# Kernel tuning notes

Hardware: AMD Instinct MI355X
Metric: run time of the kernel (lower is better)

Reference implementation:

```python
import jax, jax.numpy as jnp
import numpy as np

N = 100000      # nodes
E = 1600000     # edges (avg degree 16)
IN, H, H4, OUT = 2, 128, 32, 64
B = 1000        # batch_size for final view


def setup_inputs() -> dict:
    key = jax.random.key(0)
    ks = jax.random.split(key, 16)
    w = lambda k, s: (jax.random.normal(k, s, jnp.float32) * (1.0 / np.sqrt(s[0])))
    return {
        "x": jax.random.normal(ks[0], (N, IN), jnp.float32),
        "edge_index": jax.random.randint(ks[1], (2, E), 0, N, dtype=jnp.int32),
        "batch_size": B,
        "W1": w(ks[2], (IN, H)),  "b1": jnp.zeros((H,), jnp.float32),
        "W2": w(ks[3], (H, H)),   "b2": jnp.zeros((H,), jnp.float32),
        "W3": w(ks[4], (H, H4)),  "b3": jnp.zeros((H4,), jnp.float32),
        "W4": w(ks[5], (H4, H4)), "b4": jnp.zeros((H4,), jnp.float32),
        "W5": w(ks[6], (H4, OUT)),"b5": jnp.zeros((OUT,), jnp.float32),
        "Wl": w(ks[7], (OUT, 1)), "bl": jnp.zeros((1,), jnp.float32),
    }


def gcn_conv(x, src, dst, W, b, n):
    # PyG GCNConv: add self-loops, symmetric degree normalization, scatter-add.
    h = x @ W  # [N, F]
    deg = jax.ops.segment_sum(jnp.ones(src.shape[0], h.dtype), dst,
                              num_segments=n) + 1.0  # +1 for self-loop
    dinv = jax.lax.rsqrt(deg)  # deg >= 1, no inf
    norm = dinv[src] * dinv[dst]  # [E]
    agg = jax.ops.segment_sum(h[src] * norm[:, None], dst, num_segments=n)
    agg = agg + h * (dinv * dinv)[:, None]  # self-loop contribution
    return agg + b


def reference(x, edge_index, batch_size, W1, b1, W2, b2, W3, b3, W4, b4, W5, b5, Wl, bl):
    x = x.reshape(-1, 2)
    n = x.shape[0]
    src, dst = edge_index[0], edge_index[1]
    for W, b in ((W1, b1), (W2, b2), (W3, b3), (W4, b4), (W5, b5)):
        x = jax.nn.relu(gcn_conv(x, src, dst, W, b, n))
    x = x @ Wl + bl  # [N, 1]
    return x.reshape(batch_size, -1)
```

## Files before the change

### kernel.cpp

```cpp
#include <hip/hip_runtime.h>
#include <math.h>


static inline int cdiv(int a, int b) { return (a + b - 1) / b; }

__global__ void zero_i32(int* __restrict__ p, int n) {
    int i = blockIdx.x * 256 + threadIdx.x;
    if (i < n) p[i] = 0;
}

__global__ void count_kernel(const int* __restrict__ dst, int* __restrict__ cnt, int E) {
    int e = blockIdx.x * 256 + threadIdx.x;
    if (e < E) atomicAdd(&cnt[dst[e]], 1);
}

__global__ void scan1(const int* __restrict__ cnt, int* __restrict__ off,
                      int* __restrict__ bsum, int n) {
    __shared__ int sm[256];
    int i = blockIdx.x * 256 + threadIdx.x;
    int v = (i < n) ? cnt[i] : 0;
    sm[threadIdx.x] = v;
    __syncthreads();
    for (int ofs = 1; ofs < 256; ofs <<= 1) {
        int t = (threadIdx.x >= (unsigned)ofs) ? sm[threadIdx.x - ofs] : 0;
        __syncthreads();
        sm[threadIdx.x] += t;
        __syncthreads();
    }
    if (i < n) off[i] = sm[threadIdx.x];
    if (threadIdx.x == 255) bsum[blockIdx.x] = sm[255];
}

__global__ void scan2(const int* __restrict__ bsum, int* __restrict__ bpre,
                      int nb, int* __restrict__ off, int N, int E) {
    __shared__ int sm[512];
    int t = threadIdx.x;
    sm[t] = (t < nb) ? bsum[t] : 0;
    __syncthreads();
    for (int ofs = 1; ofs < 512; ofs <<= 1) {
        int v = (t >= ofs) ? sm[t - ofs] : 0;
        __syncthreads();
        sm[t] += v;
        __syncthreads();
    }
    if (t < nb) bpre[t] = sm[t] - bsum[t];
    if (t == 0) off[N] = E;
}

__global__ void scan3_fused(const int* __restrict__ cnt, const int* __restrict__ bpre,
                            int* __restrict__ off, int* __restrict__ cursor,
                            const float* __restrict__ x, float* __restrict__ dinv,
                            float* __restrict__ xs, int n) {
    int i = blockIdx.x * 256 + threadIdx.x;
    if (i < n) {
        int c = cnt[i];
        int o = off[i] - c + bpre[blockIdx.x];
        off[i] = o;
        cursor[i] = o;
        float dv = 1.0f / sqrtf((float)c + 1.0f);
        dinv[i] = dv;
        float2 xv = *reinterpret_cast<const float2*>(x + 2 * (size_t)i);
        *reinterpret_cast<float2*>(xs + 2 * (size_t)i) = float2{dv * xv.x, dv * xv.y};
    }
}

__global__ __launch_bounds__(256) void fill_ranged(const int* __restrict__ src,
                                                   const int* __restrict__ dst,
                                                   int* __restrict__ cursor,
                                                   int* __restrict__ csr,
                                                   int E, int N, int echunk) {
    int cls = blockIdx.x & 7;
    int chunk = blockIdx.x >> 3;
    int per = (N + 7) >> 3;
    int lo = cls * per;
    int hi = lo + per; if (hi > N) hi = N;
    int e0 = chunk * echunk;
    int e1 = e0 + echunk; if (e1 > E) e1 = E;
    for (int e = e0 + (int)threadIdx.x; e < e1; e += 256) {
        int d = dst[e];
        if (d >= lo && d < hi) {
            int p = atomicAdd(&cursor[d], 1);
            csr[p] = src[e];
        }
    }
}

__global__ __launch_bounds__(256) void agg2_kernel(const float* __restrict__ xs,
                                                   const int* __restrict__ off,
                                                   const int* __restrict__ csr,
                                                   const float* __restrict__ dinv,
                                                   float* __restrict__ out, int n) {
    int v = blockIdx.x * 256 + threadIdx.x;
    if (v >= n) return;
    float a0 = 0.f, a1 = 0.f;
    int e0 = off[v], e1 = off[v + 1];
    for (int e = e0; e < e1; e++) {
        int s = csr[e];
        float2 q = *reinterpret_cast<const float2*>(xs + 2 * (size_t)s);
        a0 += q.x;
        a1 += q.y;
    }
    float dv = dinv[v];
    float2 xv = *reinterpret_cast<const float2*>(xs + 2 * (size_t)v);
    *reinterpret_cast<float2*>(out + 2 * (size_t)v) =
        float2{dv * (a0 + xv.x), dv * (a1 + xv.y)};
}

template <bool BR, bool PS>
__global__ __launch_bounds__(256) void agg128x_kernel(const float* __restrict__ hc,
                                                      const int* __restrict__ off,
                                                      const int* __restrict__ csr,
                                                      const float* __restrict__ dinv,
                                                      const float* __restrict__ bias,
                                                      float* __restrict__ outc, int n) {
    int cls = blockIdx.x & 7;
    int chunk = cls >> 1;
    int half = cls & 1;
    int n2 = (n + 1) >> 1;
    int lo = half * n2;
    int hi = lo + n2; if (hi > n) hi = n;

    const float* __restrict__ h = hc + (size_t)chunk * n * 32;
    float* __restrict__ out = outc + (size_t)chunk * n * 32;

    int tid = threadIdx.x;
    int lane = tid & 63;
    int sl = lane & 7;
    int subbase = lane & ~7;
    int wave = tid >> 6;
    int v = lo + (blockIdx.x >> 3) * 32 + wave * 8 + (lane >> 3);
    if (v >= hi) return;

    int start = off[v];
    int end = off[v + 1];

    float4 acc = {0.f, 0.f, 0.f, 0.f};

    for (int base = start; base < end; base += 16) {
        int m = end - base;
        if (m > 16) m = 16;
        int idxA = (sl < m) ? csr[base + sl] : 0;
        int idxB = (8 + sl < m) ? csr[base + 8 + sl] : 0;
        if (m == 16) {
            float4 hb[16];
#pragma unroll
            for (int u = 0; u < 16; u++) {
                int s = __shfl((u < 8) ? idxA : idxB, subbase + (u & 7));
                hb[u] = *reinterpret_cast<const float4*>(h + (size_t)s * 32 + sl * 4);
            }
#pragma unroll
            for (int u = 0; u < 16; u++) {
                acc.x += hb[u].x; acc.y += hb[u].y; acc.z += hb[u].z; acc.w += hb[u].w;
            }
        } else {
            int ma = (m < 8) ? m : 8;
            int i = 0;
            for (; i + 4 <= ma; i += 4) {
                float4 hb[4];
#pragma unroll
                for (int u = 0; u < 4; u++) {
                    int s = __shfl(idxA, subbase + i + u);
                    hb[u] = *reinterpret_cast<const float4*>(h + (size_t)s * 32 + sl * 4);
                }
#pragma unroll
                for (int u = 0; u < 4; u++) {
                    acc.x += hb[u].x; acc.y += hb[u].y; acc.z += hb[u].z; acc.w += hb[u].w;
                }
            }
            if (i + 2 <= ma) {
                int s0 = __shfl(idxA, subbase + i);
                int s1 = __shfl(idxA, subbase + i + 1);
                float4 h0 = *reinterpret_cast<const float4*>(h + (size_t)s0 * 32 + sl * 4);
                float4 h1 = *reinterpret_cast<const float4*>(h + (size_t)s1 * 32 + sl * 4);
                acc.x += h0.x + h1.x; acc.y += h0.y + h1.y;
                acc.z += h0.z + h1.z; acc.w += h0.w + h1.w;
                i += 2;
            }
            if (i < ma) {
                int s0 = __shfl(idxA, subbase + i);
                float4 h0 = *reinterpret_cast<const float4*>(h + (size_t)s0 * 32 + sl * 4);
                acc.x += h0.x; acc.y += h0.y; acc.z += h0.z; acc.w += h0.w;
            }
            if (m > 8) {
                int mb = m - 8;
                int j = 0;
                for (; j + 4 <= mb; j += 4) {
                    float4 hb[4];
#pragma unroll
                    for (int u = 0; u < 4; u++) {
                        int s = __shfl(idxB, subbase + j + u);
                        hb[u] = *reinterpret_cast<const float4*>(h + (size_t)s * 32 + sl * 4);
                    }
#pragma unroll
                    for (int u = 0; u < 4; u++) {
                        acc.x += hb[u].x; acc.y += hb[u].y; acc.z += hb[u].z; acc.w += hb[u].w;
                    }
                }
                if (j + 2 <= mb) {
                    int s0 = __shfl(idxB, subbase + j);
                    int s1 = __shfl(idxB, subbase + j + 1);
                    float4 h0 = *reinterpret_cast<const float4*>(h + (size_t)s0 * 32 + sl * 4);
                    float4 h1 = *reinterpret_cast<const float4*>(h + (size_t)s1 * 32 + sl * 4);
                    acc.x += h0.x + h1.x; acc.y += h0.y + h1.y;
                    acc.z += h0.z + h1.z; acc.w += h0.w + h1.w;
                    j += 2;
                }
                if (j < mb) {
                    int s0 = __shfl(idxB, subbase + j);
                    float4 h0 = *reinterpret_cast<const float4*>(h + (size_t)s0 * 32 + sl * 4);
                    acc.x += h0.x; acc.y += h0.y; acc.z += h0.z; acc.w += h0.w;
                }
            }
        }
    }

    float dv = dinv[v];
    float4 hv = *reinterpret_cast<const float4*>(h + (size_t)v * 32 + sl * 4);
    float o0 = dv * (acc.x + hv.x);
    float o1 = dv * (acc.y + hv.y);
    float o2 = dv * (acc.z + hv.z);
    float o3 = dv * (acc.w + hv.w);
    if constexpr (BR) {
        float4 b = *reinterpret_cast<const float4*>(bias + chunk * 32 + sl * 4);
        o0 = fmaxf(o0 + b.x, 0.f);
        o1 = fmaxf(o1 + b.y, 0.f);
        o2 = fmaxf(o2 + b.z, 0.f);
        o3 = fmaxf(o3 + b.w, 0.f);
    }
    if constexpr (PS) {
        o0 *= dv; o1 *= dv; o2 *= dv; o3 *= dv;
    }
    *reinterpret_cast<float4*>(out + (size_t)v * 32 + sl * 4) = float4{o0, o1, o2, o3};
}

template <bool BR, bool PS>
__global__ __launch_bounds__(256) void agg32_kernel(const float* __restrict__ h,
                                                    const int* __restrict__ off,
                                                    const int* __restrict__ csr,
                                                    const float* __restrict__ dinv,
                                                    const float* __restrict__ bias,
                                                    float* __restrict__ out, int n) {
    int tid = threadIdx.x;
    int lane = tid & 63;
    int sl = lane & 7;
    int subbase = lane & ~7;
    int wave = tid >> 6;
    int v = blockIdx.x * 32 + wave * 8 + (lane >> 3);
    if (v >= n) return;

    int start = off[v];
    int end = off[v + 1];

    float4 acc = {0.f, 0.f, 0.f, 0.f};

    for (int base = start; base < end; base += 16) {
        int m = end - base;
        if (m > 16) m = 16;
        int idxA = (sl < m) ? csr[base + sl] : 0;
        int idxB = (8 + sl < m) ? csr[base + 8 + sl] : 0;
        if (m == 16) {
            float4 hb[16];
#pragma unroll
            for (int u = 0; u < 16; u++) {
                int s = __shfl((u < 8) ? idxA : idxB, subbase + (u & 7));
                hb[u] = *reinterpret_cast<const float4*>(h + (size_t)s * 32 + sl * 4);
            }
#pragma unroll
            for (int u = 0; u < 16; u++) {
                acc.x += hb[u].x; acc.y += hb[u].y; acc.z += hb[u].z; acc.w += hb[u].w;
            }
        } else {
            int ma = (m < 8) ? m : 8;
            int i = 0;
            for (; i + 4 <= ma; i += 4) {
                float4 hb[4];
#pragma unroll
                for (int u = 0; u < 4; u++) {
                    int s = __shfl(idxA, subbase + i + u);
                    hb[u] = *reinterpret_cast<const float4*>(h + (size_t)s * 32 + sl * 4);
                }
#pragma unroll
                for (int u = 0; u < 4; u++) {
                    acc.x += hb[u].x; acc.y += hb[u].y; acc.z += hb[u].z; acc.w += hb[u].w;
                }
            }
            if (i + 2 <= ma) {
                int s0 = __shfl(idxA, subbase + i);
                int s1 = __shfl(idxA, subbase + i + 1);
                float4 h0 = *reinterpret_cast<const float4*>(h + (size_t)s0 * 32 + sl * 4);
                float4 h1 = *reinterpret_cast<const float4*>(h + (size_t)s1 * 32 + sl * 4);
                acc.x += h0.x + h1.x; acc.y += h0.y + h1.y;
                acc.z += h0.z + h1.z; acc.w += h0.w + h1.w;
                i += 2;
            }
            if (i < ma) {
                int s0 = __shfl(idxA, subbase + i);
                float4 h0 = *reinterpret_cast<const float4*>(h + (size_t)s0 * 32 + sl * 4);
                acc.x += h0.x; acc.y += h0.y; acc.z += h0.z; acc.w += h0.w;
            }
            if (m > 8) {
                int mb = m - 8;
                int j = 0;
                for (; j + 4 <= mb; j += 4) {
                    float4 hb[4];
#pragma unroll
                    for (int u = 0; u < 4; u++) {
                        int s = __shfl(idxB, subbase + j + u);
                        hb[u] = *reinterpret_cast<const float4*>(h + (size_t)s * 32 + sl * 4);
                    }
#pragma unroll
                    for (int u = 0; u < 4; u++) {
                        acc.x += hb[u].x; acc.y += hb[u].y; acc.z += hb[u].z; acc.w += hb[u].w;
                    }
                }
                if (j + 2 <= mb) {
                    int s0 = __shfl(idxB, subbase + j);
                    int s1 = __shfl(idxB, subbase + j + 1);
                    float4 h0 = *reinterpret_cast<const float4*>(h + (size_t)s0 * 32 + sl * 4);
                    float4 h1 = *reinterpret_cast<const float4*>(h + (size_t)s1 * 32 + sl * 4);
                    acc.x += h0.x + h1.x; acc.y += h0.y + h1.y;
                    acc.z += h0.z + h1.z; acc.w += h0.w + h1.w;
                    j += 2;
                }
                if (j < mb) {
                    int s0 = __shfl(idxB, subbase + j);
                    float4 h0 = *reinterpret_cast<const float4*>(h + (size_t)s0 * 32 + sl * 4);
                    acc.x += h0.x; acc.y += h0.y; acc.z += h0.z; acc.w += h0.w;
                }
            }
        }
    }

    float dv = dinv[v];
    float4 hv = *reinterpret_cast<const float4*>(h + (size_t)v * 32 + sl * 4);
    float o0 = dv * (acc.x + hv.x);
    float o1 = dv * (acc.y + hv.y);
    float o2 = dv * (acc.z + hv.z);
    float o3 = dv * (acc.w + hv.w);
    if constexpr (BR) {
        float4 b = *reinterpret_cast<const float4*>(bias + sl * 4);
        o0 = fmaxf(o0 + b.x, 0.f);
        o1 = fmaxf(o1 + b.y, 0.f);
        o2 = fmaxf(o2 + b.z, 0.f);
        o3 = fmaxf(o3 + b.w, 0.f);
    }
    if constexpr (PS) {
        o0 *= dv; o1 *= dv; o2 *= dv; o3 *= dv;
    }
    *reinterpret_cast<float4*>(out + (size_t)v * 32 + sl * 4) = float4{o0, o1, o2, o3};
}

template <int K, int F, bool BR, bool PS, int CIN = 0, int COUT = 0>
__global__ __launch_bounds__(256, 4) void gemm_tiled(const float* __restrict__ x,
                                                     const float* __restrict__ W,
                                                     const float* __restrict__ bias,
                                                     const float* __restrict__ dinv,
                                                     float* __restrict__ h, int n) {
    constexpr int KC = 32;
    constexpr int KCP = 36;
    constexpr int ROWS = 64;
    constexpr int TPC = F / 4;
    constexpr int RT = 256 / TPC;
    constexpr int RPT = ROWS / RT;
    static_assert(K % KC == 0, "K must be a multiple of 32");

    __shared__ float Ws[KC * F];
    __shared__ float Xs[ROWS * KCP];

    const int tid = threadIdx.x;
    const int cb = (tid % TPC) * 4;
    const int tr = tid / TPC;
    const int row0 = blockIdx.x * ROWS;

    float acc[RPT][4];
#pragma unroll
    for (int r = 0; r < RPT; r++)
#pragma unroll
        for (int j = 0; j < 4; j++) acc[r][j] = 0.f;

#pragma unroll 1
    for (int k0 = 0; k0 < K; k0 += KC) {
        __syncthreads();
        {
            int r = tid >> 2;
            int kk = (tid & 3) * 8;
            int gr = row0 + r;
            float4 v0 = {0.f, 0.f, 0.f, 0.f}, v1 = {0.f, 0.f, 0.f, 0.f};
            if (gr < n) {
                if constexpr (CIN == 32) {
                    const float* xb = x + (size_t)(k0 >> 5) * n * 32 + (size_t)gr * 32 + kk;
                    v0 = *reinterpret_cast<const float4*>(xb);
                    v1 = *reinterpret_cast<const float4*>(xb + 4);
                } else {
                    v0 = *reinterpret_cast<const float4*>(x + (size_t)gr * K + k0 + kk);
                    v1 = *reinterpret_cast<const float4*>(x + (size_t)gr * K + k0 + kk + 4);
                }
            }
            *reinterpret_cast<float4*>(&Xs[r * KCP + kk]) = v0;
            *reinterpret_cast<float4*>(&Xs[r * KCP + kk + 4]) = v1;
        }
        for (int i = tid; i < KC * F / 4; i += 256) {
            *reinterpret_cast<float4*>(&Ws[i * 4]) =
                *reinterpret_cast<const float4*>(W + (size_t)k0 * F + i * 4);
        }
        __syncthreads();

#pragma unroll 4
        for (int kk4 = 0; kk4 < KC; kk4 += 4) {
            float4 xr[RPT];
#pragma unroll
            for (int r = 0; r < RPT; r++)
                xr[r] = *reinterpret_cast<const float4*>(&Xs[(tr * RPT + r) * KCP + kk4]);
#pragma unroll
            for (int j = 0; j < 4; j++) {
                float4 w = *reinterpret_cast<const float4*>(&Ws[(kk4 + j) * F + cb]);
#pragma unroll
                for (int r = 0; r < RPT; r++) {
                    float xv = (j == 0) ? xr[r].x : (j == 1) ? xr[r].y
                             : (j == 2) ? xr[r].z : xr[r].w;
                    acc[r][0] += xv * w.x;
                    acc[r][1] += xv * w.y;
                    acc[r][2] += xv * w.z;
                    acc[r][3] += xv * w.w;
                }
            }
        }
    }

    float4 b = float4{0.f, 0.f, 0.f, 0.f};
    if constexpr (BR) b = *reinterpret_cast<const float4*>(bias + cb);
#pragma unroll
    for (int r = 0; r < RPT; r++) {
        int row = row0 + tr * RPT + r;
        if (row < n) {
            float o0 = acc[r][0], o1 = acc[r][1], o2 = acc[r][2], o3 = acc[r][3];
            if constexpr (BR) {
                o0 = fmaxf(o0 + b.x, 0.f);
                o1 = fmaxf(o1 + b.y, 0.f);
                o2 = fmaxf(o2 + b.z, 0.f);
                o3 = fmaxf(o3 + b.w, 0.f);
            }
            if constexpr (PS) {
                float dv = dinv[row];
                o0 *= dv; o1 *= dv; o2 *= dv; o3 *= dv;
            }
            if constexpr (COUT == 32) {
                float* hb = h + (size_t)(cb >> 5) * n * 32 + (size_t)row * 32 + (cb & 31);
                *reinterpret_cast<float4*>(hb) = float4{o0, o1, o2, o3};
            } else {
                *reinterpret_cast<float4*>(&h[(size_t)row * F + cb]) = float4{o0, o1, o2, o3};
            }
        }
    }
}

__global__ __launch_bounds__(256, 4) void gemm_final(const float* __restrict__ x,
                                                     const float* __restrict__ W,
                                                     const float* __restrict__ bias,
                                                     const float* __restrict__ Wl,
                                                     const float* __restrict__ bl,
                                                     float* __restrict__ out, int n) {
    constexpr int K = 32, F = 64;
    constexpr int KC = 32;
    constexpr int KCP = 36;
    constexpr int ROWS = 64;
    constexpr int TPC = F / 4;
    constexpr int RT = 256 / TPC;
    constexpr int RPT = ROWS / RT;

    __shared__ float Ws[KC * F];
    __shared__ float Xs[ROWS * KCP];
    __shared__ float wl[F];

    const int tid = threadIdx.x;
    if (tid < F) wl[tid] = Wl[tid];
    const int cb = (tid % TPC) * 4;
    const int tr = tid / TPC;
    const int row0 = blockIdx.x * ROWS;

    float acc[RPT][4];
#pragma unroll
    for (int r = 0; r < RPT; r++)
#pragma unroll
        for (int j = 0; j < 4; j++) acc[r][j] = 0.f;

    {
        {
            int r = tid >> 2;
            int kk = (tid & 3) * 8;
            int gr = row0 + r;
            float4 v0 = {0.f, 0.f, 0.f, 0.f}, v1 = {0.f, 0.f, 0.f, 0.f};
            if (gr < n) {
                v0 = *reinterpret_cast<const float4*>(x + (size_t)gr * K + kk);
                v1 = *reinterpret_cast<const float4*>(x + (size_t)gr * K + kk + 4);
            }
            *reinterpret_cast<float4*>(&Xs[r * KCP + kk]) = v0;
            *reinterpret_cast<float4*>(&Xs[r * KCP + kk + 4]) = v1;
        }
        for (int i = tid; i < KC * F / 4; i += 256) {
            *reinterpret_cast<float4*>(&Ws[i * 4]) =
                *reinterpret_cast<const float4*>(W + i * 4);
        }
        __syncthreads();

#pragma unroll 4
        for (int kk4 = 0; kk4 < KC; kk4 += 4) {
            float4 xr[RPT];
#pragma unroll
            for (int r = 0; r < RPT; r++)
                xr[r] = *reinterpret_cast<const float4*>(&Xs[(tr * RPT + r) * KCP + kk4]);
#pragma unroll
            for (int j = 0; j < 4; j++) {
                float4 w = *reinterpret_cast<const float4*>(&Ws[(kk4 + j) * F + cb]);
#pragma unroll
                for (int r = 0; r < RPT; r++) {
                    float xv = (j == 0) ? xr[r].x : (j == 1) ? xr[r].y
                             : (j == 2) ? xr[r].z : xr[r].w;
                    acc[r][0] += xv * w.x;
                    acc[r][1] += xv * w.y;
                    acc[r][2] += xv * w.z;
                    acc[r][3] += xv * w.w;
                }
            }
        }
    }

    float4 b = *reinterpret_cast<const float4*>(bias + cb);
    float4 w = *reinterpret_cast<const float4*>(&wl[cb]);
    float blv = bl[0];
#pragma unroll
    for (int r = 0; r < RPT; r++) {
        int row = row0 + tr * RPT + r;
        float o0 = fmaxf(acc[r][0] + b.x, 0.f);
        float o1 = fmaxf(acc[r][1] + b.y, 0.f);
        float o2 = fmaxf(acc[r][2] + b.z, 0.f);
        float o3 = fmaxf(acc[r][3] + b.w, 0.f);
        float partial = o0 * w.x + o1 * w.y + o2 * w.z + o3 * w.w;
        partial += __shfl_xor(partial, 8, 16);
        partial += __shfl_xor(partial, 4, 16);
        partial += __shfl_xor(partial, 2, 16);
        partial += __shfl_xor(partial, 1, 16);
        if ((tid & 15) == 0 && row < n) out[row] = partial + blv;
    }
}

template <int K, int F, bool BR, bool PS>
__global__ __launch_bounds__(256, 4) void gemm_small(const float* __restrict__ x,
                                                     const float* __restrict__ W,
                                                     const float* __restrict__ bias,
                                                     const float* __restrict__ dinv,
                                                     float* __restrict__ h, int n) {
    constexpr int TPR = F / 4;
    constexpr int ROWS = 256 / TPR;
    __shared__ float Ws[K * F];
    for (int i = threadIdx.x; i < K * F; i += 256) Ws[i] = W[i];
    __syncthreads();

    int tid = threadIdx.x;
    int cb = (tid % TPR) * 4;
    int r = blockIdx.x * ROWS + tid / TPR;
    if (r >= n) return;

    const float* xr = x + (size_t)r * K;
    float a0 = 0.f, a1 = 0.f, a2 = 0.f, a3 = 0.f;
#pragma unroll
    for (int k = 0; k < K; k++) {
        float xv = xr[k];
        float4 w = *reinterpret_cast<const float4*>(&Ws[k * F + cb]);
        a0 += xv * w.x; a1 += xv * w.y; a2 += xv * w.z; a3 += xv * w.w;
    }
    if constexpr (BR) {
        float4 b = *reinterpret_cast<const float4*>(bias + cb);
        a0 = fmaxf(a0 + b.x, 0.f);
        a1 = fmaxf(a1 + b.y, 0.f);
        a2 = fmaxf(a2 + b.z, 0.f);
        a3 = fmaxf(a3 + b.w, 0.f);
    }
    if constexpr (PS) {
        float dv = dinv[r];
        a0 *= dv; a1 *= dv; a2 *= dv; a3 *= dv;
    }
    *reinterpret_cast<float4*>(&h[(size_t)r * F + cb]) = float4{a0, a1, a2, a3};
}

extern "C" void kernel_launch(void* const* d_in, const int* in_sizes, int n_in,
                              void* d_out, int out_size, void* d_ws, size_t ws_size,
                              hipStream_t stream) {
    const float* x = (const float*)d_in[0];
    const int* ei = (const int*)d_in[1];
    const float* W1 = (const float*)d_in[3];
    const float* b1 = (const float*)d_in[4];
    const float* W2 = (const float*)d_in[5];
    const float* b2 = (const float*)d_in[6];
    const float* W3 = (const float*)d_in[7];
    const float* b3 = (const float*)d_in[8];
    const float* W4 = (const float*)d_in[9];
    const float* b4 = (const float*)d_in[10];
    const float* W5 = (const float*)d_in[11];
    const float* b5 = (const float*)d_in[12];
    const float* Wl = (const float*)d_in[13];
    const float* bl = (const float*)d_in[14];

    const int N = in_sizes[0] / 2;
    const int E = in_sizes[1] / 2;
    const int* src = ei;
    const int* dst = ei + E;

    char* wp = (char*)d_ws;
    auto alloc = [&](size_t bytes) -> void* {
        void* p = wp;
        wp += ((bytes + 255) / 256) * 256;
        return p;
    };
    int* cnt = (int*)alloc((size_t)N * 4);
    int* off = (int*)alloc((size_t)(N + 1) * 4);
    int* cursor = (int*)alloc((size_t)N * 4);
    int* bsum = (int*)alloc(512 * 4);
    int* bpre = (int*)alloc(512 * 4);
    int* csr = (int*)alloc((size_t)E * 4);
    float* dinv = (float*)alloc((size_t)N * 4);
    float* xs2 = (float*)alloc((size_t)N * 2 * 4);
    float* t2 = (float*)alloc((size_t)N * 2 * 4);
    float* bufA = (float*)alloc((size_t)N * 128 * 4);
    float* bufB = (float*)alloc((size_t)N * 128 * 4);

    const int gN = cdiv(N, 256);
    const int gE = cdiv(E, 256);
    const int nb = gN;
    const int gT = cdiv(N, 64);

    const int NCHUNK = 128;
    const int echunk = cdiv(E, NCHUNK);
    const int gR = 8 * NCHUNK;

    const int gX = 8 * cdiv((N + 1) / 2, 32);

    zero_i32<<<gN, 256, 0, stream>>>(cnt, N);
    count_kernel<<<gE, 256, 0, stream>>>(dst, cnt, E);
    scan1<<<nb, 256, 0, stream>>>(cnt, off, bsum, N);
    scan2<<<1, 512, 0, stream>>>(bsum, bpre, nb, off, N, E);
    scan3_fused<<<nb, 256, 0, stream>>>(cnt, bpre, off, cursor, x, dinv, xs2, N);
    fill_ranged<<<gR, 256, 0, stream>>>(src, dst, cursor, csr, E, N, echunk);

    agg2_kernel<<<gN, 256, 0, stream>>>(xs2, off, csr, dinv, t2, N);
    gemm_small<2, 128, true, true><<<cdiv(N, 8), 256, 0, stream>>>(t2, W1, b1, dinv, bufA, N);
    gemm_tiled<128, 128, false, false, 0, 32><<<gT, 256, 0, stream>>>(bufA, W2, nullptr, nullptr, bufB, N);
    agg128x_kernel<true, true><<<gX, 256, 0, stream>>>(bufB, off, csr, dinv, b2, bufA, N);
    gemm_tiled<128, 32, false, false, 32, 0><<<gT, 256, 0, stream>>>(bufA, W3, nullptr, nullptr, bufB, N);
    agg32_kernel<true, true><<<cdiv(N, 32), 256, 0, stream>>>(bufB, off, csr, dinv, b3, bufA, N);
    gemm_tiled<32, 32, false, false, 0, 0><<<gT, 256, 0, stream>>>(bufA, W4, nullptr, nullptr, bufB, N);
    agg32_kernel<true, true><<<cdiv(N, 32), 256, 0, stream>>>(bufB, off, csr, dinv, b4, bufA, N);
    agg32_kernel<false, false><<<cdiv(N, 32), 256, 0, stream>>>(bufA, off, csr, dinv, nullptr, bufB, N);
    gemm_final<<<gT, 256, 0, stream>>>(bufB, W5, b5, Wl, bl, (float*)d_out, N);
}
```

Measured before the change: 530.5 us.

## Split 32-wide feature layers into 8-column chunks for cache-friendly aggregation

Stores the 32-feature hidden activations as four column chunks of 8 floats each (chunk-major), and rewrites the 32-wide aggregation to process one chunk per block class, also splitting nodes into halves. Each gather then touches a 32-byte row inside a 3.2 MB chunk array instead of a 12.8 MB array, aiming to keep the gathered working set in cache. This mirrors the earlier 128-wide chunked kernel. The GEMMs gain matching chunked input and output addressing. The cost is four times as many narrower scalar gathers per edge, and the CSR indices are re-read once per chunk.

Measured after the change: 572.3 us. 1.08x slower.

```diff
diff --git a/kernel.cpp b/kernel.cpp
--- a/kernel.cpp
+++ b/kernel.cpp
@@ -234,24 +234,34 @@
 }
 
 template <bool BR, bool PS>
-__global__ __launch_bounds__(256) void agg32_kernel(const float* __restrict__ h,
-                                                    const int* __restrict__ off,
-                                                    const int* __restrict__ csr,
-                                                    const float* __restrict__ dinv,
-                                                    const float* __restrict__ bias,
-                                                    float* __restrict__ out, int n) {
+__global__ __launch_bounds__(256) void agg32x_kernel(const float* __restrict__ hc,
+                                                     const int* __restrict__ off,
+                                                     const int* __restrict__ csr,
+                                                     const float* __restrict__ dinv,
+                                                     const float* __restrict__ bias,
+                                                     float* __restrict__ outc, int n) {
+    int cls = blockIdx.x & 7;
+    int chunk = cls >> 1;
+    int half = cls & 1;
+    int n2 = (n + 1) >> 1;
+    int lo = half * n2;
+    int hi = lo + n2; if (hi > n) hi = n;
+
+    const float* __restrict__ h = hc + (size_t)chunk * n * 8;
+    float* __restrict__ out = outc + (size_t)chunk * n * 8;
+
     int tid = threadIdx.x;
     int lane = tid & 63;
     int sl = lane & 7;
     int subbase = lane & ~7;
     int wave = tid >> 6;
-    int v = blockIdx.x * 32 + wave * 8 + (lane >> 3);
-    if (v >= n) return;
+    int v = lo + (blockIdx.x >> 3) * 32 + wave * 8 + (lane >> 3);
+    if (v >= hi) return;
 
     int start = off[v];
     int end = off[v + 1];
 
-    float4 acc = {0.f, 0.f, 0.f, 0.f};
+    float acc = 0.f;
 
     for (int base = start; base < end; base += 16) {
         int m = end - base;
@@ -259,95 +269,74 @@
         int idxA = (sl < m) ? csr[base + sl] : 0;
         int idxB = (8 + sl < m) ? csr[base + 8 + sl] : 0;
         if (m == 16) {
-            float4 hb[16];
+            float hb[16];
 #pragma unroll
             for (int u = 0; u < 16; u++) {
                 int s = __shfl((u < 8) ? idxA : idxB, subbase + (u & 7));
-                hb[u] = *reinterpret_cast<const float4*>(h + (size_t)s * 32 + sl * 4);
-            }
-#pragma unroll
-            for (int u = 0; u < 16; u++) {
-                acc.x += hb[u].x; acc.y += hb[u].y; acc.z += hb[u].z; acc.w += hb[u].w;
-            }
+                hb[u] = h[(size_t)s * 8 + sl];
+            }
+#pragma unroll
+            for (int u = 0; u < 16; u++) acc += hb[u];
         } else {
             int ma = (m < 8) ? m : 8;
             int i = 0;
             for (; i + 4 <= ma; i += 4) {
-                float4 hb[4];
+                float hb[4];
 #pragma unroll
                 for (int u = 0; u < 4; u++) {
                     int s = __shfl(idxA, subbase + i + u);
-                    hb[u] = *reinterpret_cast<const float4*>(h + (size_t)s * 32 + sl * 4);
-                }
-#pragma unroll
-                for (int u = 0; u < 4; u++) {
-                    acc.x += hb[u].x; acc.y += hb[u].y; acc.z += hb[u].z; acc.w += hb[u].w;
-                }
+                    hb[u] = h[(size_t)s * 8 + sl];
+                }
+#pragma unroll
+                for (int u = 0; u < 4; u++) acc += hb[u];
             }
             if (i + 2 <= ma) {
                 int s0 = __shfl(idxA, subbase + i);
                 int s1 = __shfl(idxA, subbase + i + 1);
-                float4 h0 = *reinterpret_cast<const float4*>(h + (size_t)s0 * 32 + sl * 4);
-                float4 h1 = *reinterpret_cast<const float4*>(h + (size_t)s1 * 32 + sl * 4);
-                acc.x += h0.x + h1.x; acc.y += h0.y + h1.y;
-                acc.z += h0.z + h1.z; acc.w += h0.w + h1.w;
+                acc += h[(size_t)s0 * 8 + sl] + h[(size_t)s1 * 8 + sl];
                 i += 2;
             }
             if (i < ma) {
                 int s0 = __shfl(idxA, subbase + i);
-                float4 h0 = *reinterpret_cast<const float4*>(h + (size_t)s0 * 32 + sl * 4);
-                acc.x += h0.x; acc.y += h0.y; acc.z += h0.z; acc.w += h0.w;
+                acc += h[(size_t)s0 * 8 + sl];
             }
             if (m > 8) {
                 int mb = m - 8;
                 int j = 0;
                 for (; j + 4 <= mb; j += 4) {
-                    float4 hb[4];
+                    float hb[4];
 #pragma unroll
                     for (int u = 0; u < 4; u++) {
                         int s = __shfl(idxB, subbase + j + u);
-                        hb[u] = *reinterpret_cast<const float4*>(h + (size_t)s * 32 + sl * 4);
+                        hb[u] = h[(size_t)s * 8 + sl];
                     }
 #pragma unroll
-                    for (int u = 0; u < 4; u++) {
-                        acc.x += hb[u].x; acc.y += hb[u].y; acc.z += hb[u].z; acc.w += hb[u].w;
-                    }
+                    for (int u = 0; u < 4; u++) acc += hb[u];
                 }
                 if (j + 2 <= mb) {
                     int s0 = __shfl(idxB, subbase + j);
                     int s1 = __shfl(idxB, subbase + j + 1);
-                    float4 h0 = *reinterpret_cast<const float4*>(h + (size_t)s0 * 32 + sl * 4);
-                    float4 h1 = *reinterpret_cast<const float4*>(h + (size_t)s1 * 32 + sl * 4);
-                    acc.x += h0.x + h1.x; acc.y += h0.y + h1.y;
-                    acc.z += h0.z + h1.z; acc.w += h0.w + h1.w;
+                    acc += h[(size_t)s0 * 8 + sl] + h[(size_t)s1 * 8 + sl];
                     j += 2;
                 }
                 if (j < mb) {
                     int s0 = __shfl(idxB, subbase + j);
-                    float4 h0 = *reinterpret_cast<const float4*>(h + (size_t)s0 * 32 + sl * 4);
-                    acc.x += h0.x; acc.y += h0.y; acc.z += h0.z; acc.w += h0.w;
+                    acc += h[(size_t)s0 * 8 + sl];
                 }
             }
         }
     }
 
     float dv = dinv[v];
-    float4 hv = *reinterpret_cast<const float4*>(h + (size_t)v * 32 + sl * 4);
-    float o0 = dv * (acc.x + hv.x);
-    float o1 = dv * (acc.y + hv.y);
-    float o2 = dv * (acc.z + hv.z);
-    float o3 = dv * (acc.w + hv.w);
+    float hv = h[(size_t)v * 8 + sl];
+    float o = dv * (acc + hv);
     if constexpr (BR) {
-        float4 b = *reinterpret_cast<const float4*>(bias + sl * 4);
-        o0 = fmaxf(o0 + b.x, 0.f);
-        o1 = fmaxf(o1 + b.y, 0.f);
-        o2 = fmaxf(o2 + b.z, 0.f);
-        o3 = fmaxf(o3 + b.w, 0.f);
+        o = fmaxf(o + bias[chunk * 8 + sl], 0.f);
     }
     if constexpr (PS) {
-        o0 *= dv; o1 *= dv; o2 *= dv; o3 *= dv;
-    }
-    *reinterpret_cast<float4*>(out + (size_t)v * 32 + sl * 4) = float4{o0, o1, o2, o3};
+        o *= dv;
+    }
+    out[(size_t)v * 8 + sl] = o;
 }
 
 template <int K, int F, bool BR, bool PS, int CIN = 0, int COUT = 0>
@@ -391,6 +380,10 @@
                     const float* xb = x + (size_t)(k0 >> 5) * n * 32 + (size_t)gr * 32 + kk;
                     v0 = *reinterpret_cast<const float4*>(xb);
                     v1 = *reinterpret_cast<const float4*>(xb + 4);
+                } else if constexpr (CIN == 8) {
+                    const float* xb = x + (size_t)((k0 + kk) >> 3) * n * 8 + (size_t)gr * 8;
+                    v0 = *reinterpret_cast<const float4*>(xb);
+                    v1 = *reinterpret_cast<const float4*>(xb + 4);
                 } else {
                     v0 = *reinterpret_cast<const float4*>(x + (size_t)gr * K + k0 + kk);
                     v1 = *reinterpret_cast<const float4*>(x + (size_t)gr * K + k0 + kk + 4);
@@ -446,6 +439,9 @@
             }
             if constexpr (COUT == 32) {
                 float* hb = h + (size_t)(cb >> 5) * n * 32 + (size_t)row * 32 + (cb & 31);
+                *reinterpret_cast<float4*>(hb) = float4{o0, o1, o2, o3};
+            } else if constexpr (COUT == 8) {
+                float* hb = h + (size_t)(cb >> 3) * n * 8 + (size_t)row * 8 + (cb & 7);
                 *reinterpret_cast<float4*>(hb) = float4{o0, o1, o2, o3};
             } else {
                 *reinterpret_cast<float4*>(&h[(size_t)row * F + cb]) = float4{o0, o1, o2, o3};
@@ -491,8 +487,9 @@
             int gr = row0 + r;
             float4 v0 = {0.f, 0.f, 0.f, 0.f}, v1 = {0.f, 0.f, 0.f, 0.f};
             if (gr < n) {
-                v0 = *reinterpret_cast<const float4*>(x + (size_t)gr * K + kk);
-                v1 = *reinterpret_cast<const float4*>(x + (size_t)gr * K + kk + 4);
+                const float* xb = x + (size_t)(kk >> 3) * n * 8 + (size_t)gr * 8;
+                v0 = *reinterpret_cast<const float4*>(xb);
+                v1 = *reinterpret_cast<const float4*>(xb + 4);
             }
             *reinterpret_cast<float4*>(&Xs[r * KCP + kk]) = v0;
             *reinterpret_cast<float4*>(&Xs[r * KCP + kk + 4]) = v1;
@@ -646,10 +643,10 @@
     gemm_small<2, 128, true, true><<<cdiv(N, 8), 256, 0, stream>>>(t2, W1, b1, dinv, bufA, N);
     gemm_tiled<128, 128, false, false, 0, 32><<<gT, 256, 0, stream>>>(bufA, W2, nullptr, nullptr, bufB, N);
     agg128x_kernel<true, true><<<gX, 256, 0, stream>>>(bufB, off, csr, dinv, b2, bufA, N);
-    gemm_tiled<128, 32, false, false, 32, 0><<<gT, 256, 0, stream>>>(bufA, W3, nullptr, nullptr, bufB, N);
-    agg32_kernel<true, true><<<cdiv(N, 32), 256, 0, stream>>>(bufB, off, csr, dinv, b3, bufA, N);
-    gemm_tiled<32, 32, false, false, 0, 0><<<gT, 256, 0, stream>>>(bufA, W4, nullptr, nullptr, bufB, N);
-    agg32_kernel<true, true><<<cdiv(N, 32), 256, 0, stream>>>(bufB, off, csr, dinv, b4, bufA, N);
-    agg32_kernel<false, false><<<cdiv(N, 32), 256, 0, stream>>>(bufA, off, csr, dinv, nullptr, bufB, N);
+    gemm_tiled<128, 32, false, false, 32, 8><<<gT, 256, 0, stream>>>(bufA, W3, nullptr, nullptr, bufB, N);
+    agg32x_kernel<true, true><<<gX, 256, 0, stream>>>(bufB, off, csr, dinv, b3, bufA, N);
+    gemm_tiled<32, 32, false, false, 8, 8><<<gT, 256, 0, stream>>>(bufA, W4, nullptr, nullptr, bufB, N);
+    agg32x_kernel<true, true><<<gX, 256, 0, stream>>>(bufB, off, csr, dinv, b4, bufA, N);
+    agg32x_kernel<false, false><<<gX, 256, 0, stream>>>(bufA, off, csr, dinv, nullptr, bufB, N);
     gemm_final<<<gT, 256, 0, stream>>>(bufB, W5, b5, Wl, bl, (float*)d_out, N);
 }
```

## Partition CSR neighbors into source octants for phased L2-local gathers in agg128

Applied to the files above, without the earlier changes.

The CSR build now buckets each destination's neighbors by which eighth of the node range their source falls in, using per-node 8-way counters and cursors. The 128-wide aggregation kernel uses these buckets to sweep the octants in order, with each 8-lane group handling 9 nodes at once. The goal is to keep the gathered source rows for the current phase inside a smaller working set that fits in cache. The cost is 8x larger count and cursor arrays, more atomics and scan work, shorter 4-wide inner batches with less memory-level parallelism per node, and higher register pressure.

Result: slower. 630.4 us (+18.8%).

```diff
diff --git a/kernel.cpp b/kernel.cpp
--- a/kernel.cpp
+++ b/kernel.cpp
@@ -9,16 +9,27 @@
     if (i < n) p[i] = 0;
 }
 
-__global__ void count_kernel(const int* __restrict__ dst, int* __restrict__ cnt, int E) {
+__global__ void count_q8(const int* __restrict__ src, const int* __restrict__ dst,
+                         int* __restrict__ cnt8, int E, int q1) {
     int e = blockIdx.x * 256 + threadIdx.x;
-    if (e < E) atomicAdd(&cnt[dst[e]], 1);
-}
-
-__global__ void scan1(const int* __restrict__ cnt, int* __restrict__ off,
-                      int* __restrict__ bsum, int n) {
+    if (e < E) {
+        int s = src[e];
+        int q = (s >= q1) + (s >= 2 * q1) + (s >= 3 * q1) + (s >= 4 * q1) +
+                (s >= 5 * q1) + (s >= 6 * q1) + (s >= 7 * q1);
+        atomicAdd(&cnt8[dst[e] * 8 + q], 1);
+    }
+}
+
+__global__ void scan1q8(const int* __restrict__ cnt8, int* __restrict__ off,
+                        int* __restrict__ bsum, int n) {
     __shared__ int sm[256];
     int i = blockIdx.x * 256 + threadIdx.x;
-    int v = (i < n) ? cnt[i] : 0;
+    int v = 0;
+    if (i < n) {
+        int4 a = *reinterpret_cast<const int4*>(cnt8 + 8 * (size_t)i);
+        int4 b = *reinterpret_cast<const int4*>(cnt8 + 8 * (size_t)i + 4);
+        v = a.x + a.y + a.z + a.w + b.x + b.y + b.z + b.w;
+    }
     sm[threadIdx.x] = v;
     __syncthreads();
     for (int ofs = 1; ofs < 256; ofs <<= 1) {
@@ -47,16 +58,28 @@
     if (t == 0) off[N] = E;
 }
 
-__global__ void scan3_fused(const int* __restrict__ cnt, const int* __restrict__ bpre,
-                            int* __restrict__ off, int* __restrict__ cursor,
-                            const float* __restrict__ x, float* __restrict__ dinv,
-                            float* __restrict__ xs, int n) {
+__global__ void scan3_fused8(const int* __restrict__ cnt8, const int* __restrict__ bpre,
+                             int* __restrict__ off, int* __restrict__ cur8,
+                             const float* __restrict__ x, float* __restrict__ dinv,
+                             float* __restrict__ xs, int n) {
     int i = blockIdx.x * 256 + threadIdx.x;
     if (i < n) {
-        int c = cnt[i];
+        int4 a = *reinterpret_cast<const int4*>(cnt8 + 8 * (size_t)i);
+        int4 b = *reinterpret_cast<const int4*>(cnt8 + 8 * (size_t)i + 4);
+        int c = a.x + a.y + a.z + a.w + b.x + b.y + b.z + b.w;
         int o = off[i] - c + bpre[blockIdx.x];
         off[i] = o;
-        cursor[i] = o;
+        int4 ca, cb;
+        ca.x = o;
+        ca.y = ca.x + a.x;
+        ca.z = ca.y + a.y;
+        ca.w = ca.z + a.z;
+        cb.x = ca.w + a.w;
+        cb.y = cb.x + b.x;
+        cb.z = cb.y + b.y;
+        cb.w = cb.z + b.z;
+        *reinterpret_cast<int4*>(cur8 + 8 * (size_t)i) = ca;
+        *reinterpret_cast<int4*>(cur8 + 8 * (size_t)i + 4) = cb;
         float dv = 1.0f / sqrtf((float)c + 1.0f);
         dinv[i] = dv;
         float2 xv = *reinterpret_cast<const float2*>(x + 2 * (size_t)i);
@@ -64,11 +87,11 @@
     }
 }
 
-__global__ __launch_bounds__(256) void fill_ranged(const int* __restrict__ src,
-                                                   const int* __restrict__ dst,
-                                                   int* __restrict__ cursor,
-                                                   int* __restrict__ csr,
-                                                   int E, int N, int echunk) {
+__global__ __launch_bounds__(256) void fill_ranged8(const int* __restrict__ src,
+                                                    const int* __restrict__ dst,
+                                                    int* __restrict__ cur8,
+                                                    int* __restrict__ csr,
+                                                    int E, int N, int echunk, int q1) {
     int cls = blockIdx.x & 7;
     int chunk = blockIdx.x >> 3;
     int per = (N + 7) >> 3;
@@ -79,8 +102,11 @@
     for (int e = e0 + (int)threadIdx.x; e < e1; e += 256) {
         int d = dst[e];
         if (d >= lo && d < hi) {
-            int p = atomicAdd(&cursor[d], 1);
-            csr[p] = src[e];
+            int s = src[e];
+            int q = (s >= q1) + (s >= 2 * q1) + (s >= 3 * q1) + (s >= 4 * q1) +
+                    (s >= 5 * q1) + (s >= 6 * q1) + (s >= 7 * q1);
+            int p = atomicAdd(&cur8[d * 8 + q], 1);
+            csr[p] = s;
         }
     }
 }
@@ -106,13 +132,14 @@
         float2{dv * (a0 + xv.x), dv * (a1 + xv.y)};
 }
 
-template <bool BR, bool PS>
-__global__ __launch_bounds__(256) void agg128x_kernel(const float* __restrict__ hc,
-                                                      const int* __restrict__ off,
-                                                      const int* __restrict__ csr,
-                                                      const float* __restrict__ dinv,
-                                                      const float* __restrict__ bias,
-                                                      float* __restrict__ outc, int n) {
+template <bool BR, bool PS, int NG>
+__global__ __launch_bounds__(256, 6) void agg128xp_kernel(const float* __restrict__ hc,
+                                                          const int* __restrict__ off,
+                                                          const int* __restrict__ cur8,
+                                                          const int* __restrict__ csr,
+                                                          const float* __restrict__ dinv,
+                                                          const float* __restrict__ bias,
+                                                          float* __restrict__ outc, int n) {
     int cls = blockIdx.x & 7;
     int chunk = cls >> 1;
     int half = cls & 1;
@@ -127,110 +154,80 @@
     int lane = tid & 63;
     int sl = lane & 7;
     int subbase = lane & ~7;
-    int wave = tid >> 6;
-    int v = lo + (blockIdx.x >> 3) * 32 + wave * 8 + (lane >> 3);
-    if (v >= hi) return;
-
-    int start = off[v];
-    int end = off[v + 1];
-
-    float4 acc = {0.f, 0.f, 0.f, 0.f};
-
-    for (int base = start; base < end; base += 16) {
-        int m = end - base;
-        if (m > 16) m = 16;
-        int idxA = (sl < m) ? csr[base + sl] : 0;
-        int idxB = (8 + sl < m) ? csr[base + 8 + sl] : 0;
-        if (m == 16) {
-            float4 hb[16];
-#pragma unroll
-            for (int u = 0; u < 16; u++) {
-                int s = __shfl((u < 8) ? idxA : idxB, subbase + (u & 7));
-                hb[u] = *reinterpret_cast<const float4*>(h + (size_t)s * 32 + sl * 4);
-            }
-#pragma unroll
-            for (int u = 0; u < 16; u++) {
-                acc.x += hb[u].x; acc.y += hb[u].y; acc.z += hb[u].z; acc.w += hb[u].w;
-            }
-        } else {
-            int ma = (m < 8) ? m : 8;
-            int i = 0;
-            for (; i + 4 <= ma; i += 4) {
-                float4 hb[4];
-#pragma unroll
-                for (int u = 0; u < 4; u++) {
-                    int s = __shfl(idxA, subbase + i + u);
-                    hb[u] = *reinterpret_cast<const float4*>(h + (size_t)s * 32 + sl * 4);
-                }
-#pragma unroll
-                for (int u = 0; u < 4; u++) {
-                    acc.x += hb[u].x; acc.y += hb[u].y; acc.z += hb[u].z; acc.w += hb[u].w;
-                }
-            }
-            if (i + 2 <= ma) {
-                int s0 = __shfl(idxA, subbase + i);
-                int s1 = __shfl(idxA, subbase + i + 1);
-                float4 h0 = *reinterpret_cast<const float4*>(h + (size_t)s0 * 32 + sl * 4);
-                float4 h1 = *reinterpret_cast<const float4*>(h + (size_t)s1 * 32 + sl * 4);
-                acc.x += h0.x + h1.x; acc.y += h0.y + h1.y;
-                acc.z += h0.z + h1.z; acc.w += h0.w + h1.w;
-                i += 2;
-            }
-            if (i < ma) {
-                int s0 = __shfl(idxA, subbase + i);
-                float4 h0 = *reinterpret_cast<const float4*>(h + (size_t)s0 * 32 + sl * 4);
-                acc.x += h0.x; acc.y += h0.y; acc.z += h0.z; acc.w += h0.w;
-            }
-            if (m > 8) {
-                int mb = m - 8;
-                int j = 0;
-                for (; j + 4 <= mb; j += 4) {
+    int grpid = tid >> 3;
+    int nstart = lo + (blockIdx.x >> 3) * (NG * 32);
+
+    float4 acc[NG];
+#pragma unroll
+    for (int g = 0; g < NG; g++) acc[g] = float4{0.f, 0.f, 0.f, 0.f};
+
+#pragma unroll 1
+    for (int q = 0; q < 8; q++) {
+#pragma unroll
+        for (int g = 0; g < NG; g++) {
+            int v = nstart + g * 32 + grpid;
+            if (v >= hi) continue;
+            int s0 = (q == 0) ? off[v] : cur8[v * 8 + q - 1];
+            int s1 = cur8[v * 8 + q];
+            for (int base = s0; base < s1; base += 4) {
+                int m = s1 - base; if (m > 4) m = 4;
+                int idx = (sl < m) ? csr[base + sl] : 0;
+                if (m == 4) {
                     float4 hb[4];
 #pragma unroll
                     for (int u = 0; u < 4; u++) {
-                        int s = __shfl(idxB, subbase + j + u);
+                        int s = __shfl(idx, subbase + u);
                         hb[u] = *reinterpret_cast<const float4*>(h + (size_t)s * 32 + sl * 4);
                     }
 #pragma unroll
                     for (int u = 0; u < 4; u++) {
-                        acc.x += hb[u].x; acc.y += hb[u].y; acc.z += hb[u].z; acc.w += hb[u].w;
+                        acc[g].x += hb[u].x; acc[g].y += hb[u].y;
+                        acc[g].z += hb[u].z; acc[g].w += hb[u].w;
                     }
-                }
-                if (j + 2 <= mb) {
-                    int s0 = __shfl(idxB, subbase + j);
-                    int s1 = __shfl(idxB, subbase + j + 1);
-                    float4 h0 = *reinterpret_cast<const float4*>(h + (size_t)s0 * 32 + sl * 4);
-                    float4 h1 = *reinterpret_cast<const float4*>(h + (size_t)s1 * 32 + sl * 4);
-                    acc.x += h0.x + h1.x; acc.y += h0.y + h1.y;
-                    acc.z += h0.z + h1.z; acc.w += h0.w + h1.w;
-                    j += 2;
-                }
-                if (j < mb) {
-                    int s0 = __shfl(idxB, subbase + j);
-                    float4 h0 = *reinterpret_cast<const float4*>(h + (size_t)s0 * 32 + sl * 4);
-                    acc.x += h0.x; acc.y += h0.y; acc.z += h0.z; acc.w += h0.w;
-                }
-            }
-        }
-    }
-
-    float dv = dinv[v];
-    float4 hv = *reinterpret_cast<const float4*>(h + (size_t)v * 32 + sl * 4);
-    float o0 = dv * (acc.x + hv.x);
-    float o1 = dv * (acc.y + hv.y);
-    float o2 = dv * (acc.z + hv.z);
-    float o3 = dv * (acc.w + hv.w);
-    if constexpr (BR) {
-        float4 b = *reinterpret_cast<const float4*>(bias + chunk * 32 + sl * 4);
-        o0 = fmaxf(o0 + b.x, 0.f);
-        o1 = fmaxf(o1 + b.y, 0.f);
-        o2 = fmaxf(o2 + b.z, 0.f);
-        o3 = fmaxf(o3 + b.w, 0.f);
-    }
-    if constexpr (PS) {
-        o0 *= dv; o1 *= dv; o2 *= dv; o3 *= dv;
-    }
-    *reinterpret_cast<float4*>(out + (size_t)v * 32 + sl * 4) = float4{o0, o1, o2, o3};
+                } else {
+                    int i = 0;
+                    if (i + 2 <= m) {
+                        int sa = __shfl(idx, subbase + i);
+                        int sb = __shfl(idx, subbase + i + 1);
+                        float4 h0 = *reinterpret_cast<const float4*>(h + (size_t)sa * 32 + sl * 4);
+                        float4 h1 = *reinterpret_cast<const float4*>(h + (size_t)sb * 32 + sl * 4);
+                        acc[g].x += h0.x + h1.x; acc[g].y += h0.y + h1.y;
+                        acc[g].z += h0.z + h1.z; acc[g].w += h0.w + h1.w;
+                        i += 2;
+                    }
+                    if (i < m) {
+                        int sa = __shfl(idx, subbase + i);
+                        float4 h0 = *reinterpret_cast<const float4*>(h + (size_t)sa * 32 + sl * 4);
+                        acc[g].x += h0.x; acc[g].y += h0.y;
+                        acc[g].z += h0.z; acc[g].w += h0.w;
+                    }
+                }
+            }
+        }
+    }
+
+#pragma unroll
+    for (int g = 0; g < NG; g++) {
+        int v = nstart + g * 32 + grpid;
+        if (v >= hi) continue;
+        float dv = dinv[v];
+        float4 hv = *reinterpret_cast<const float4*>(h + (size_t)v * 32 + sl * 4);
+        float o0 = dv * (acc[g].x + hv.x);
+        float o1 = dv * (acc[g].y + hv.y);
+        float o2 = dv * (acc[g].z + hv.z);
+        float o3 = dv * (acc[g].w + hv.w);
+        if constexpr (BR) {
+            float4 b = *reinterpret_cast<const float4*>(bias + chunk * 32 + sl * 4);
+            o0 = fmaxf(o0 + b.x, 0.f);
+            o1 = fmaxf(o1 + b.y, 0.f);
+            o2 = fmaxf(o2 + b.z, 0.f);
+            o3 = fmaxf(o3 + b.w, 0.f);
+        }
+        if constexpr (PS) {
+            o0 *= dv; o1 *= dv; o2 *= dv; o3 *= dv;
+        }
+        *reinterpret_cast<float4*>(out + (size_t)v * 32 + sl * 4) = float4{o0, o1, o2, o3};
+    }
 }
 
 template <bool BR, bool PS>
@@ -612,9 +609,9 @@
         wp += ((bytes + 255) / 256) * 256;
         return p;
     };
-    int* cnt = (int*)alloc((size_t)N * 4);
+    int* cnt8 = (int*)alloc((size_t)N * 8 * 4);
     int* off = (int*)alloc((size_t)(N + 1) * 4);
-    int* cursor = (int*)alloc((size_t)N * 4);
+    int* cur8 = (int*)alloc((size_t)N * 8 * 4);
     int* bsum = (int*)alloc(512 * 4);
     int* bpre = (int*)alloc(512 * 4);
     int* csr = (int*)alloc((size_t)E * 4);
@@ -628,24 +625,27 @@
     const int gE = cdiv(E, 256);
     const int nb = gN;
     const int gT = cdiv(N, 64);
+    const int q1 = cdiv(N, 8);
 
     const int NCHUNK = 128;
     const int echunk = cdiv(E, NCHUNK);
     const int gR = 8 * NCHUNK;
 
-    const int gX = 8 * cdiv((N + 1) / 2, 32);
-
-    zero_i32<<<gN, 256, 0, stream>>>(cnt, N);
-    count_kernel<<<gE, 256, 0, stream>>>(dst, cnt, E);
-    scan1<<<nb, 256, 0, stream>>>(cnt, off, bsum, N);
+    constexpr int NG = 9;
+    const int BPC = cdiv((N + 1) / 2, NG * 32);
+    const int gP = 8 * BPC;
+
+    zero_i32<<<cdiv(8 * N, 256), 256, 0, stream>>>(cnt8, 8 * N);
+    count_q8<<<gE, 256, 0, stream>>>(src, dst, cnt8, E, q1);
+    scan1q8<<<nb, 256, 0, stream>>>(cnt8, off, bsum, N);
     scan2<<<1, 512, 0, stream>>>(bsum, bpre, nb, off, N, E);
-    scan3_fused<<<nb, 256, 0, stream>>>(cnt, bpre, off, cursor, x, dinv, xs2, N);
-    fill_ranged<<<gR, 256, 0, stream>>>(src, dst, cursor, csr, E, N, echunk);
+    scan3_fused8<<<nb, 256, 0, stream>>>(cnt8, bpre, off, cur8, x, dinv, xs2, N);
+    fill_ranged8<<<gR, 256, 0, stream>>>(src, dst, cur8, csr, E, N, echunk, q1);
 
     agg2_kernel<<<gN, 256, 0, stream>>>(xs2, off, csr, dinv, t2, N);
     gemm_small<2, 128, true, true><<<cdiv(N, 8), 256, 0, stream>>>(t2, W1, b1, dinv, bufA, N);
     gemm_tiled<128, 128, false, false, 0, 32><<<gT, 256, 0, stream>>>(bufA, W2, nullptr, nullptr, bufB, N);
-    agg128x_kernel<true, true><<<gX, 256, 0, stream>>>(bufB, off, csr, dinv, b2, bufA, N);
+    agg128xp_kernel<true, true, NG><<<gP, 256, 0, stream>>>(bufB, off, cur8, csr, dinv, b2, bufA, N);
     gemm_tiled<128, 32, false, false, 32, 0><<<gT, 256, 0, stream>>>(bufA, W3, nullptr, nullptr, bufB, N);
     agg32_kernel<true, true><<<cdiv(N, 32), 256, 0, stream>>>(bufB, off, csr, dinv, b3, bufA, N);
     gemm_tiled<32, 32, false, false, 0, 0><<<gT, 256, 0, stream>>>(bufA, W4, nullptr, nullptr, bufB, N);
```
